# Performance work log

Measured on AMD Instinct MI355X. Metric: run time of the kernel, lower is better.

The kernel has to match this reference:

```python
import jax, jax.numpy as jnp
import numpy as np

B, N, DH = 256, 32, 128      # batch, n_agents, per-agent hidden
E = 496                       # n_edges (fully connected over 32 agents)
DIM_IN = 2 * DH               # 256, MLP input (concat of two agent states)
DIM_HID = 256
A = 12                        # dim_act
R = 4                         # payoff_rank
DIM_OUT = 2 * R * A           # 96


def setup_inputs() -> dict:
    key = jax.random.key(0)
    ks = jax.random.split(key, 7)
    hidden_states_n = jax.random.normal(ks[0], (B, N, DH), dtype=jnp.float32)
    edges_from = jax.random.randint(ks[1], (E,), 0, N, dtype=jnp.int32).astype(jnp.int64)
    edges_to = jax.random.randint(ks[2], (E,), 0, N, dtype=jnp.int32).astype(jnp.int64)
    # torch.nn.Linear params: W [out, in], b [out]
    W1 = jax.random.normal(ks[3], (DIM_HID, DIM_IN), dtype=jnp.float32) * (1.0 / np.sqrt(DIM_IN))
    b1 = jnp.zeros((DIM_HID,), dtype=jnp.float32)
    W2 = jax.random.normal(ks[4], (DIM_OUT, DIM_HID), dtype=jnp.float32) * (1.0 / np.sqrt(DIM_HID))
    b2 = jnp.zeros((DIM_OUT,), dtype=jnp.float32)
    return {"hidden_states_n": hidden_states_n, "W1": W1, "b1": b1, "W2": W2,
            "b2": b2, "edges_from": edges_from, "edges_to": edges_to}


def reference(hidden_states_n, W1, b1, W2, b2, edges_from, edges_to):
    hf = hidden_states_n[:, edges_from]                     # [B, E, DH]
    ht = hidden_states_n[:, edges_to]                       # [B, E, DH]
    # stack of (from||to, to||from): [2, B, E, 2*DH]
    inp = jnp.stack([jnp.concatenate([hf, ht], axis=-1),
                     jnp.concatenate([ht, hf], axis=-1)], axis=0)
    h = jax.nn.relu(inp @ W1.T + b1)                        # [2, B, E, DIM_HID]
    p = h @ W2.T + b2                                       # [2, B, E, 2*R*A]
    p = p.reshape(2, B, E, R, 2, A)
    # low-rank outer product per rank, summed over ranks: [2, B, E, A, A]
    payoffs = jnp.einsum('sberi,sberj->sbeij', p[..., 0, :], p[..., 1, :])
    # second copy is transposed, then mean over the two directions
    return 0.5 * (payoffs[0] + jnp.swapaxes(payoffs[1], -1, -2))  # [B, E, A, A]
```

## Files before the change

### kernel.cpp

```cpp
#include <hip/hip_runtime.h>

typedef unsigned int uint;
typedef _Float16 f16;

typedef __attribute__((ext_vector_type(8))) _Float16 f16x8;
typedef __attribute__((ext_vector_type(2))) _Float16 f16x2;
typedef __attribute__((ext_vector_type(4))) float f32x4;

#define E_CNT 496

#define W2_STRIDE 136
#define W2_HALF_F16 (96 * W2_STRIDE)
#define W2_HALF_BYTES (W2_HALF_F16 * 2)
#define W2_CHUNKS 26
#define LDS_BYTES 26624

#define PP_STRIDE 136
#define V_OFF 1088
#define PW_F16 2176

__device__ __forceinline__ uint pack2_f16(float lo, float hi) {
    union { f16x2 h; uint u; } r;
    r.h[0] = (_Float16)lo;
    r.h[1] = (_Float16)hi;
    return r.u;
}

__device__ __forceinline__ void load_lds16(const void* g, void* l) {
    __builtin_amdgcn_global_load_lds(
        (const __attribute__((address_space(1))) void*)g,
        (__attribute__((address_space(3))) void*)l, 16, 0, 0);
}

__global__ __launch_bounds__(256) void x_kernel(
    const float* __restrict__ hidden, const float* __restrict__ W1,
    const float* __restrict__ b1, f16* __restrict__ Xout,
    const float* __restrict__ W2, f16* __restrict__ w2h) {
    __shared__ __align__(16) float hs[64 * 132];

    const int tid = threadIdx.x;

    if (blockIdx.x == 512) {
        #pragma unroll
        for (int j = 0; j < 24; ++j) {
            int idx4 = tid + j * 256;
            int n = idx4 >> 6;
            int k = (idx4 & 63) << 2;
            int h = k >> 7;
            int kin = k & 127;
            float4 v = *(const float4*)&W2[n * 256 + k];
            uint2 o;
            o.x = pack2_f16(v.x, v.y);
            o.y = pack2_f16(v.z, v.w);
            *(uint2*)&w2h[h * W2_HALF_F16 + n * W2_STRIDE + kin] = o;
        }
        return;
    }

    const int rowblock = blockIdx.x >> 2;
    const int g = blockIdx.x & 3;
    const int ln = tid & 63;
    const int waveId = tid >> 6;
    const int quad = ln >> 4;
    const int l16 = ln & 15;
    const int row0 = rowblock * 64;

    union FU { uint u[4]; f16x8 v; };
    FU wf[2][4];
    float bh[2][4];
    #pragma unroll
    for (int nt = 0; nt < 2; ++nt) {
        const int t = (g * 4 + waveId) * 2 + nt;
        const int half = t >> 4;
        const int htile = t & 15;
        const float* wrow = W1 + (htile * 16 + l16) * 256 + half * 128 + quad * 8;
        #pragma unroll
        for (int kk = 0; kk < 4; ++kk) {
            float4 v0 = *(const float4*)(wrow + kk * 32);
            float4 v1 = *(const float4*)(wrow + kk * 32 + 4);
            wf[nt][kk].u[0] = pack2_f16(v0.x, v0.y);
            wf[nt][kk].u[1] = pack2_f16(v0.z, v0.w);
            wf[nt][kk].u[2] = pack2_f16(v1.x, v1.y);
            wf[nt][kk].u[3] = pack2_f16(v1.z, v1.w);
        }
        #pragma unroll
        for (int r = 0; r < 4; ++r)
            bh[nt][r] = 0.5f * b1[htile * 16 + quad * 4 + r];
    }

    {
        const float* src = hidden + row0 * 128;
        #pragma unroll
        for (int it = 0; it < 8; ++it) {
            int idx = it * 256 + tid;
            int r = idx >> 5;
            int c4 = idx & 31;
            float4 v = *(const float4*)(src + idx * 4);
            *(float4*)&hs[r * 132 + c4 * 4] = v;
        }
    }
    __syncthreads();

    #pragma unroll
    for (int ch = 0; ch < 4; ++ch) {
        FU hf[4];
        const float* hrow = &hs[(ch * 16 + l16) * 132 + quad * 8];
        #pragma unroll
        for (int kk = 0; kk < 4; ++kk) {
            float4 v0 = *(const float4*)(hrow + kk * 32);
            float4 v1 = *(const float4*)(hrow + kk * 32 + 4);
            hf[kk].u[0] = pack2_f16(v0.x, v0.y);
            hf[kk].u[1] = pack2_f16(v0.z, v0.w);
            hf[kk].u[2] = pack2_f16(v1.x, v1.y);
            hf[kk].u[3] = pack2_f16(v1.z, v1.w);
        }
        #pragma unroll
        for (int nt = 0; nt < 2; ++nt) {
            const int t = (g * 4 + waveId) * 2 + nt;
            const int half = t >> 4;
            const int htile = t & 15;
            f32x4 acc = (f32x4){0.f, 0.f, 0.f, 0.f};
            #pragma unroll
            for (int kk = 0; kk < 4; ++kk)
                acc = __builtin_amdgcn_mfma_f32_16x16x32_f16(wf[nt][kk].v, hf[kk].v, acc, 0, 0, 0);
            uint2 o;
            o.x = pack2_f16(acc[0] + bh[nt][0], acc[1] + bh[nt][1]);
            o.y = pack2_f16(acc[2] + bh[nt][2], acc[3] + bh[nt][3]);
            f16* dst = Xout + half * (8192 * 256)
                     + (row0 + ch * 16 + l16) * 256 + htile * 16 + quad * 4;
            *(uint2*)dst = o;
        }
    }
}

__global__ __launch_bounds__(256) void gemm_payoff_kernel(
    const f16* __restrict__ X1, const f16* __restrict__ X2,
    const int* __restrict__ e_f, const int* __restrict__ e_t,
    const f16* __restrict__ w2g, const float* __restrict__ b2,
    float* __restrict__ out) {

    __shared__ __align__(16) unsigned char smem[LDS_BYTES];
    f16* w2s = (f16*)smem;

    const int tid = threadIdx.x;
    const int ln = tid & 63;
    const int waveId = tid >> 6;
    const int quad = ln >> 4;
    const int l16 = ln & 15;
    const int pl = l16 & 7;
    const int s = l16 >> 3;

    const int bx = blockIdx.x;
    const int lb = (bx & 7) * 248 + (bx >> 3);

    auto stageW2 = [&](int h) {
        const unsigned char* src = (const unsigned char*)w2g + h * W2_HALF_BYTES + ln * 16;
        #pragma unroll
        for (int j = 0; j < 7; ++j) {
            int i = waveId + j * 4;
            if (i < W2_CHUNKS)
                load_lds16(src + i * 1024, smem + i * 1024);
        }
    };

    stageW2(0);

    bool f64 = true, t64 = true;
    #pragma unroll
    for (int i = 0; i < 16; ++i) {
        if (e_f[2 * i + 1] != 0) f64 = false;
        if (e_t[2 * i + 1] != 0) t64 = false;
    }

    const int pairBase = lb * 64 + waveId * 16;
    const f16* px1[2];
    const f16* px2[2];
    #pragma unroll
    for (int mt = 0; mt < 2; ++mt) {
        int pair = pairBase + mt * 8 + pl;
        int b = pair / E_CNT;
        int e = pair - b * E_CNT;
        int f = f64 ? e_f[2 * e] : e_f[e];
        int t = t64 ? e_t[2 * e] : e_t[e];
        int n1 = s ? t : f;
        int n2 = s ? f : t;
        px1[mt] = X1 + ((b * 32 + n1) * 256 + quad * 8);
        px2[mt] = X2 + ((b * 32 + n2) * 256 + quad * 8);
    }

    float b2v[6];
    #pragma unroll
    for (int tt = 0; tt < 6; ++tt) b2v[tt] = b2[tt * 16 + l16];

    int d6[6];
    float psc[6];
    {
        const int s_ = quad >> 1;
        #pragma unroll
        for (int tt = 0; tt < 6; ++tt) {
            int n = tt * 16 + l16;
            int rr = n / 24;
            int rem = n - rr * 24;
            int c01 = (rem >= 12) ? 1 : 0;
            int a = rem - c01 * 12;
            int k8 = s_ * 4 + rr;
            int toL = (c01 == s_) ? 1 : 0;
            d6[tt] = (toL ? 0 : V_OFF) + (quad & 1) * 4 * PP_STRIDE + a * 8 + k8;
            psc[tt] = toL ? 0.5f : 1.0f;
        }
    }

    const f16x8 zero8 = (f16x8){0, 0, 0, 0, 0, 0, 0, 0};
    f16* pm = (f16*)smem + waveId * PW_F16;

    typedef union { uint4 q; f16x8 h; } XU;

    #pragma unroll
    for (int mt = 0; mt < 2; ++mt) {
        f32x4 acc[6];
        #pragma unroll
        for (int tt = 0; tt < 6; ++tt) acc[tt] = (f32x4){0.f, 0.f, 0.f, 0.f};

        XU G1[2], G2[2];
        G1[0].q = *(const uint4*)(px1[mt] + 0 * 32);
        G2[0].q = *(const uint4*)(px2[mt] + 0 * 32);
        G1[1].q = *(const uint4*)(px1[mt] + 1 * 32);
        G2[1].q = *(const uint4*)(px2[mt] + 1 * 32);

        __syncthreads();

        #pragma unroll
        for (int kk = 0; kk < 4; ++kk) {
            const int buf = kk & 1;
            f16x8 sum = G1[buf].h + G2[buf].h;
            f16x8 af = __builtin_elementwise_max(sum, zero8);
            G1[buf].q = *(const uint4*)(px1[mt] + (kk + 2) * 32);
            G2[buf].q = *(const uint4*)(px2[mt] + (kk + 2) * 32);
            #pragma unroll
            for (int tt = 0; tt < 6; ++tt) {
                f16x8 bf = *(const f16x8*)&w2s[(tt * 16 + l16) * W2_STRIDE + kk * 32 + quad * 8];
                acc[tt] = __builtin_amdgcn_mfma_f32_16x16x32_f16(af, bf, acc[tt], 0, 0, 0);
            }
        }

        __syncthreads();
        stageW2(1);
        __syncthreads();

        #pragma unroll
        for (int kk = 4; kk < 8; ++kk) {
            const int buf = kk & 1;
            f16x8 sum = G1[buf].h + G2[buf].h;
            f16x8 af = __builtin_elementwise_max(sum, zero8);
            if (kk < 6) {
                G1[buf].q = *(const uint4*)(px1[mt] + (kk + 2) * 32);
                G2[buf].q = *(const uint4*)(px2[mt] + (kk + 2) * 32);
            }
            #pragma unroll
            for (int tt = 0; tt < 6; ++tt) {
                f16x8 bf = *(const f16x8*)&w2s[(tt * 16 + l16) * W2_STRIDE + (kk - 4) * 32 + quad * 8];
                acc[tt] = __builtin_amdgcn_mfma_f32_16x16x32_f16(af, bf, acc[tt], 0, 0, 0);
            }
        }

        __syncthreads();

        #pragma unroll
        for (int tt = 0; tt < 6; ++tt) {
            #pragma unroll
            for (int r = 0; r < 4; ++r)
                pm[d6[tt] + r * PP_STRIDE] = (_Float16)((acc[tt][r] + b2v[tt]) * psc[tt]);
        }

        #pragma unroll
        for (int pp = 0; pp < 8; ++pp) {
            f16x8 afp = zero8, bfp = zero8;
            if (quad == 0) {
                afp = *(const f16x8*)&pm[V_OFF + pp * PP_STRIDE + l16 * 8];
                bfp = *(const f16x8*)&pm[pp * PP_STRIDE + l16 * 8];
            }
            f32x4 d = __builtin_amdgcn_mfma_f32_16x16x32_f16(
                afp, bfp, (f32x4){0.f, 0.f, 0.f, 0.f}, 0, 0, 0);
            if (l16 < 12 && quad < 3) {
                float* ob = out + (pairBase + mt * 8 + pp) * 144 + l16 * 12 + quad * 4;
                *(float4*)ob = make_float4(d[0], d[1], d[2], d[3]);
            }
        }

        if (mt == 0) {
            __syncthreads();
            stageW2(0);
        }
    }
}

extern "C" void kernel_launch(void* const* d_in, const int* in_sizes, int n_in,
                              void* d_out, int out_size, void* d_ws, size_t ws_size,
                              hipStream_t stream) {
    const float* hidden = (const float*)d_in[0];
    const float* W1 = (const float*)d_in[1];
    const float* b1 = (const float*)d_in[2];
    const float* W2 = (const float*)d_in[3];
    const float* b2 = (const float*)d_in[4];
    const int* e_f = (const int*)d_in[5];
    const int* e_t = (const int*)d_in[6];
    float* out = (float*)d_out;

    char* ws = (char*)d_ws;
    f16* X = (f16*)ws;
    f16* w2h = (f16*)(ws + 8 * 1024 * 1024);

    x_kernel<<<513, 256, 0, stream>>>(hidden, W1, b1, X, W2, w2h);
    gemm_payoff_kernel<<<1984, 256, 0, stream>>>(X, X + 8192 * 256, e_f, e_t, w2h, b2, out);
}
```

Before: 136.4 us.

## Stage full W2 in LDS once and use 512-thread blocks, one m-tile per wave

The GEMM-payoff kernel now holds the entire fp16 W2 (both K halves, padded stride 264) in LDS and loads it once per block. This replaces the earlier scheme of restaging each half twice per block with barriers in between. Blocks grow to 8 waves, each handling 8 edge pairs instead of two sequential 8-pair tiles, which removes the per-tile restage syncs and increases parallelism per block. LDS use roughly doubles to about 51 KB per block, which may cut how many blocks fit on a CU.

```diff
diff --git a/kernel.cpp b/kernel.cpp
--- a/kernel.cpp
+++ b/kernel.cpp
@@ -9,11 +9,11 @@
 
 #define E_CNT 496
 
-#define W2_STRIDE 136
-#define W2_HALF_F16 (96 * W2_STRIDE)
-#define W2_HALF_BYTES (W2_HALF_F16 * 2)
-#define W2_CHUNKS 26
-#define LDS_BYTES 26624
+#define W2_STRIDE 264
+#define W2_F16 (96 * W2_STRIDE)
+#define W2_STAGE_BYTES 52224
+#define W2_CHUNKS 51
+#define LDS_BYTES 52224
 
 #define PP_STRIDE 136
 #define V_OFF 1088
@@ -46,13 +46,11 @@
             int idx4 = tid + j * 256;
             int n = idx4 >> 6;
             int k = (idx4 & 63) << 2;
-            int h = k >> 7;
-            int kin = k & 127;
             float4 v = *(const float4*)&W2[n * 256 + k];
             uint2 o;
             o.x = pack2_f16(v.x, v.y);
             o.y = pack2_f16(v.z, v.w);
-            *(uint2*)&w2h[h * W2_HALF_F16 + n * W2_STRIDE + kin] = o;
+            *(uint2*)&w2h[n * W2_STRIDE + k] = o;
         }
         return;
     }
@@ -133,7 +131,7 @@
     }
 }
 
-__global__ __launch_bounds__(256) void gemm_payoff_kernel(
+__global__ __launch_bounds__(512) void gemm_payoff_kernel(
     const f16* __restrict__ X1, const f16* __restrict__ X2,
     const int* __restrict__ e_f, const int* __restrict__ e_t,
     const f16* __restrict__ w2g, const float* __restrict__ b2,
@@ -153,17 +151,15 @@
     const int bx = blockIdx.x;
     const int lb = (bx & 7) * 248 + (bx >> 3);
 
-    auto stageW2 = [&](int h) {
-        const unsigned char* src = (const unsigned char*)w2g + h * W2_HALF_BYTES + ln * 16;
+    {
+        const unsigned char* src = (const unsigned char*)w2g + ln * 16;
         #pragma unroll
         for (int j = 0; j < 7; ++j) {
-            int i = waveId + j * 4;
+            int i = waveId + j * 8;
             if (i < W2_CHUNKS)
                 load_lds16(src + i * 1024, smem + i * 1024);
         }
-    };
-
-    stageW2(0);
+    }
 
     bool f64 = true, t64 = true;
     #pragma unroll
@@ -172,20 +168,19 @@
         if (e_t[2 * i + 1] != 0) t64 = false;
     }
 
-    const int pairBase = lb * 64 + waveId * 16;
-    const f16* px1[2];
-    const f16* px2[2];
-    #pragma unroll
-    for (int mt = 0; mt < 2; ++mt) {
-        int pair = pairBase + mt * 8 + pl;
+    const int pairBase = lb * 64 + waveId * 8;
+    const f16* px1;
+    const f16* px2;
+    {
+        int pair = pairBase + pl;
         int b = pair / E_CNT;
         int e = pair - b * E_CNT;
         int f = f64 ? e_f[2 * e] : e_f[e];
         int t = t64 ? e_t[2 * e] : e_t[e];
         int n1 = s ? t : f;
         int n2 = s ? f : t;
-        px1[mt] = X1 + ((b * 32 + n1) * 256 + quad * 8);
-        px2[mt] = X2 + ((b * 32 + n2) * 256 + quad * 8);
+        px1 = X1 + ((b * 32 + n1) * 256 + quad * 8);
+        px2 = X2 + ((b * 32 + n2) * 256 + quad * 8);
     }
 
     float b2v[6];
@@ -210,86 +205,60 @@
         }
     }
 
+    f32x4 acc[6];
+    #pragma unroll
+    for (int tt = 0; tt < 6; ++tt) acc[tt] = (f32x4){0.f, 0.f, 0.f, 0.f};
+
+    typedef union { uint4 q; f16x8 h; } XU;
+    XU G1[2], G2[2];
+    G1[0].q = *(const uint4*)(px1 + 0 * 32);
+    G2[0].q = *(const uint4*)(px2 + 0 * 32);
+    G1[1].q = *(const uint4*)(px1 + 1 * 32);
+    G2[1].q = *(const uint4*)(px2 + 1 * 32);
+
     const f16x8 zero8 = (f16x8){0, 0, 0, 0, 0, 0, 0, 0};
+
+    __syncthreads();
+
+    #pragma unroll
+    for (int kk = 0; kk < 8; ++kk) {
+        const int buf = kk & 1;
+        f16x8 sum = G1[buf].h + G2[buf].h;
+        f16x8 af = __builtin_elementwise_max(sum, zero8);
+        if (kk < 6) {
+            G1[buf].q = *(const uint4*)(px1 + (kk + 2) * 32);
+            G2[buf].q = *(const uint4*)(px2 + (kk + 2) * 32);
+        }
+        #pragma unroll
+        for (int tt = 0; tt < 6; ++tt) {
+            f16x8 bf = *(const f16x8*)&w2s[(tt * 16 + l16) * W2_STRIDE + kk * 32 + quad * 8];
+            acc[tt] = __builtin_amdgcn_mfma_f32_16x16x32_f16(af, bf, acc[tt], 0, 0, 0);
+        }
+    }
+
+    __syncthreads();
+
     f16* pm = (f16*)smem + waveId * PW_F16;
 
-    typedef union { uint4 q; f16x8 h; } XU;
-
-    #pragma unroll
-    for (int mt = 0; mt < 2; ++mt) {
-        f32x4 acc[6];
-        #pragma unroll
-        for (int tt = 0; tt < 6; ++tt) acc[tt] = (f32x4){0.f, 0.f, 0.f, 0.f};
-
-        XU G1[2], G2[2];
-        G1[0].q = *(const uint4*)(px1[mt] + 0 * 32);
-        G2[0].q = *(const uint4*)(px2[mt] + 0 * 32);
-        G1[1].q = *(const uint4*)(px1[mt] + 1 * 32);
-        G2[1].q = *(const uint4*)(px2[mt] + 1 * 32);
-
-        __syncthreads();
-
-        #pragma unroll
-        for (int kk = 0; kk < 4; ++kk) {
-            const int buf = kk & 1;
-            f16x8 sum = G1[buf].h + G2[buf].h;
-            f16x8 af = __builtin_elementwise_max(sum, zero8);
-            G1[buf].q = *(const uint4*)(px1[mt] + (kk + 2) * 32);
-            G2[buf].q = *(const uint4*)(px2[mt] + (kk + 2) * 32);
-            #pragma unroll
-            for (int tt = 0; tt < 6; ++tt) {
-                f16x8 bf = *(const f16x8*)&w2s[(tt * 16 + l16) * W2_STRIDE + kk * 32 + quad * 8];
-                acc[tt] = __builtin_amdgcn_mfma_f32_16x16x32_f16(af, bf, acc[tt], 0, 0, 0);
-            }
-        }
-
-        __syncthreads();
-        stageW2(1);
-        __syncthreads();
-
-        #pragma unroll
-        for (int kk = 4; kk < 8; ++kk) {
-            const int buf = kk & 1;
-            f16x8 sum = G1[buf].h + G2[buf].h;
-            f16x8 af = __builtin_elementwise_max(sum, zero8);
-            if (kk < 6) {
-                G1[buf].q = *(const uint4*)(px1[mt] + (kk + 2) * 32);
-                G2[buf].q = *(const uint4*)(px2[mt] + (kk + 2) * 32);
-            }
-            #pragma unroll
-            for (int tt = 0; tt < 6; ++tt) {
-                f16x8 bf = *(const f16x8*)&w2s[(tt * 16 + l16) * W2_STRIDE + (kk - 4) * 32 + quad * 8];
-                acc[tt] = __builtin_amdgcn_mfma_f32_16x16x32_f16(af, bf, acc[tt], 0, 0, 0);
-            }
-        }
-
-        __syncthreads();
-
-        #pragma unroll
-        for (int tt = 0; tt < 6; ++tt) {
-            #pragma unroll
-            for (int r = 0; r < 4; ++r)
-                pm[d6[tt] + r * PP_STRIDE] = (_Float16)((acc[tt][r] + b2v[tt]) * psc[tt]);
-        }
-
-        #pragma unroll
-        for (int pp = 0; pp < 8; ++pp) {
-            f16x8 afp = zero8, bfp = zero8;
-            if (quad == 0) {
-                afp = *(const f16x8*)&pm[V_OFF + pp * PP_STRIDE + l16 * 8];
-                bfp = *(const f16x8*)&pm[pp * PP_STRIDE + l16 * 8];
-            }
-            f32x4 d = __builtin_amdgcn_mfma_f32_16x16x32_f16(
-                afp, bfp, (f32x4){0.f, 0.f, 0.f, 0.f}, 0, 0, 0);
-            if (l16 < 12 && quad < 3) {
-                float* ob = out + (pairBase + mt * 8 + pp) * 144 + l16 * 12 + quad * 4;
-                *(float4*)ob = make_float4(d[0], d[1], d[2], d[3]);
-            }
-        }
-
-        if (mt == 0) {
-            __syncthreads();
-            stageW2(0);
+    #pragma unroll
+    for (int tt = 0; tt < 6; ++tt) {
+        #pragma unroll
+        for (int r = 0; r < 4; ++r)
+            pm[d6[tt] + r * PP_STRIDE] = (_Float16)((acc[tt][r] + b2v[tt]) * psc[tt]);
+    }
+
+    #pragma unroll
+    for (int pp = 0; pp < 8; ++pp) {
+        f16x8 afp = zero8, bfp = zero8;
+        if (quad == 0) {
+            afp = *(const f16x8*)&pm[V_OFF + pp * PP_STRIDE + l16 * 8];
+            bfp = *(const f16x8*)&pm[pp * PP_STRIDE + l16 * 8];
+        }
+        f32x4 d = __builtin_amdgcn_mfma_f32_16x16x32_f16(
+            afp, bfp, (f32x4){0.f, 0.f, 0.f, 0.f}, 0, 0, 0);
+        if (l16 < 12 && quad < 3) {
+            float* ob = out + (pairBase + pp) * 144 + l16 * 12 + quad * 4;
+            *(float4*)ob = make_float4(d[0], d[1], d[2], d[3]);
         }
     }
 }
@@ -311,5 +280,5 @@
     f16* w2h = (f16*)(ws + 8 * 1024 * 1024);
 
     x_kernel<<<513, 256, 0, stream>>>(hidden, W1, b1, X, W2, w2h);
-    gemm_payoff_kernel<<<1984, 256, 0, stream>>>(X, X + 8192 * 256, e_f, e_t, w2h, b2, out);
-}
+    gemm_payoff_kernel<<<1984, 512, 0, stream>>>(X, X + 8192 * 256, e_f, e_t, w2h, b2, out);
+}
```

Result: faster. 131.6 us (-3.5%).
